# Performance work log

Hardware: AMD Instinct MI355X
Metric: run time of the kernel (lower is better)

Reference implementation:

```python
import jax, jax.numpy as jnp
import numpy as np

B, S, H, OUT = 64, 513, 1024, 128   # batch, seq (incl CLS), hidden, slot labels
T = S - 1                            # subword tokens after dropping [CLS]
P_WORD_START = 0.75                  # avg ~1.33 subwords per word


def setup_inputs() -> dict:
    key = jax.random.key(0)
    k1, k2, k3, k4 = jax.random.split(key, 4)
    hidden_states = jax.random.normal(k1, (B, S, H), jnp.float32)
    W = jax.random.normal(k2, (H, OUT), jnp.float32) * 0.02
    b = jax.random.normal(k3, (OUT,), jnp.float32) * 0.02
    # contiguous, non-decreasing word ids: cumsum of word-start flags
    starts = (jax.random.uniform(k4, (B, T)) < P_WORD_START).astype(jnp.int32)
    starts = starts.at[:, 0].set(1)
    segment_ids = jnp.cumsum(starts, axis=-1) - 1  # [B, T], values in [0, n_words)
    return {"hidden_states": hidden_states, "W": W, "b": b,
            "segment_ids": segment_ids}


def _merge_row(logits, seg):
    # logits: [T, OUT], seg: [T] contiguous non-decreasing word ids
    s = jax.ops.segment_sum(logits, seg, num_segments=T)                    # [T, OUT]
    c = jax.ops.segment_sum(jnp.ones((T,), logits.dtype), seg, num_segments=T)
    mean = s / jnp.maximum(c, 1.0)[:, None]
    # words beyond n_words (empty segments) -> zero padding, as in the original
    return jnp.where(c[:, None] > 0, mean, 0.0)


def reference(hidden_states, W, b, segment_ids):
    x = hidden_states[:, 1:]                       # drop [CLS]; dropout = identity (eval)
    logits = jnp.einsum('bth,ho->bto', x, W) + b   # [B, T, OUT]
    merged = jax.vmap(_merge_row)(logits, segment_ids)  # per-word ragged mean + pad
    return jnp.transpose(merged, (0, 2, 1))        # [B, OUT, T]
```

## Files before the change

### kernel.cpp

```cpp
#include <hip/hip_runtime.h>
#include <hip/hip_bf16.h>

#define B_    64
#define S_    513
#define T_    512
#define H_    1024
#define OUT_  128
#define OWN   64
#define ROWS  96
#define HP    512
#define NKK   16

typedef __attribute__((ext_vector_type(8))) short short8_t;
typedef __attribute__((ext_vector_type(4))) float f32x4;

__device__ inline ushort f2bf(float f) {
    union { float f; unsigned u; } x; x.f = f;
    unsigned r = x.u + 0x7fffu + ((x.u >> 16) & 1u);
    return (ushort)(r >> 16);
}

__global__ __launch_bounds__(256) void wt_kernel(
    const float* __restrict__ W, ushort* __restrict__ Wt)
{
    __shared__ ushort tile[64][65];
    int k0 = blockIdx.x * 64, o0 = blockIdx.y * 64;
    int tid = threadIdx.x;
#pragma unroll
    for (int p = 0; p < 16; ++p) {
        int idx = tid + p * 256;
        int r = idx >> 6, c = idx & 63;
        tile[r][c] = f2bf(W[(size_t)(k0 + r) * OUT_ + o0 + c]);
    }
    __syncthreads();
#pragma unroll
    for (int p = 0; p < 16; ++p) {
        int idx = tid + p * 256;
        int c = idx >> 6, r = idx & 63;
        Wt[(size_t)(o0 + c) * H_ + k0 + r] = tile[r][c];
    }
}

__global__ __launch_bounds__(512, 4) void fused_kernel(
    const float* __restrict__ hs, const ushort* __restrict__ Wt,
    const float* __restrict__ bias, const int* __restrict__ seg,
    float* __restrict__ out)
{
    __shared__ ushort sums[32768];
    __shared__ int sseg[ROWS];
    __shared__ int lcnt[OWN];
    __shared__ int sExt, sSlo;

    int bid  = blockIdx.x;
    int b    = bid >> 3;
    int tile = bid & 7;
    int t0   = tile * OWN;
    int Tl   = (T_ - t0) < ROWS ? (T_ - t0) : ROWS;

    int tid  = threadIdx.x;
    int lane = tid & 63;
    int w    = tid >> 6;
    int wm   = w & 1, wn = w >> 1;
    int l15  = lane & 15, ksl = lane >> 4;

    if (tid < Tl)  sseg[tid] = seg[b * T_ + t0 + tid];
    if (tid < OWN) lcnt[tid] = 0;
    if (tid == 0)  sExt = Tl;
    __syncthreads();
    if (tid == 0) {
        bool start0 = (t0 == 0) || (seg[b * T_ + t0 - 1] != sseg[0]);
        sSlo = sseg[0] + (start0 ? 0 : 1);
    }
    if (tid >= OWN && tid < Tl && sseg[tid] != sseg[tid - 1])
        atomicMin(&sExt, tid);
    __syncthreads();
    int ext  = sExt;
    int s_lo = sSlo;
    int s_hi = sseg[OWN - 1] + 1;
    int ns   = s_hi - s_lo;
    if (tid < ext) {
        int sid = sseg[tid] - s_lo;
        if (sid >= 0) atomicAdd(&lcnt[sid], 1);
    }
    __syncthreads();

    const float* xcol = hs + ((size_t)(b * S_ + 1 + t0)) * H_ + tid;
    const ushort* bp0 = Wt + (size_t)(wn * 32 + l15) * H_ + ksl * 8;
    const ushort* bp1 = bp0 + (size_t)16 * H_;
    int widx   = ((tid >> 3) << 9) + (tid & 7);
    int rbase0 = ksl * 512 + (wm * 32 + l15) * 8;
    int rbase1 = rbase0 + 16 * 8;

    f32x4 acc[2][2];
#pragma unroll
    for (int fm = 0; fm < 2; ++fm)
#pragma unroll
        for (int fn = 0; fn < 2; ++fn) acc[fm][fn] = (f32x4){0.f, 0.f, 0.f, 0.f};

    for (int pass = 0; pass < 2; ++pass) {
        const float* xp = xcol + pass * HP;
        int cur = -1; float racc = 0.f;
        float va[8], vc[8];

        auto LOADC = [&](float (&v)[8], int tb) {
#pragma unroll
            for (int i = 0; i < 8; ++i) {
                int t = tb + i; t = t < Tl ? t : Tl - 1;
                v[i] = xp[(size_t)t * H_];
            }
        };
        auto PROC = [&](float (&v)[8], int tb) {
#pragma unroll
            for (int i = 0; i < 8; ++i) {
                int t = tb + i;
                if (t < ext) {
                    int sid = sseg[t] - s_lo;
                    if (sid >= 0) {
                        if (sid != cur) {
                            if (cur >= 0) sums[widx + (cur << 3)] = f2bf(racc);
                            cur = sid; racc = v[i];
                        } else {
                            racc += v[i];
                        }
                    }
                }
            }
        };

        LOADC(va, 0);
        for (int tb = 0; ; tb += 16) {
            LOADC(vc, tb + 8);
            PROC(va, tb);
            if (tb + 8 >= ext) break;
            LOADC(va, tb + 16);
            PROC(vc, tb + 8);
            if (tb + 16 >= ext) break;
        }
        if (cur >= 0) sums[widx + (cur << 3)] = f2bf(racc);
        __syncthreads();

        const ushort* bq0 = bp0 + pass * HP;
        const ushort* bq1 = bp1 + pass * HP;
        short8_t bfA[2], bfB[2];

        auto LB2 = [&](short8_t (&d)[2], int kk) {
            d[0] = *reinterpret_cast<const short8_t*>(bq0 + kk * 32);
            d[1] = *reinterpret_cast<const short8_t*>(bq1 + kk * 32);
        };
        auto STEP = [&](int kk, short8_t (&bf)[2]) {
            short8_t a0 = *reinterpret_cast<const short8_t*>(&sums[rbase0 + kk * 2048]);
            short8_t a1 = *reinterpret_cast<const short8_t*>(&sums[rbase1 + kk * 2048]);
            acc[0][0] = __builtin_amdgcn_mfma_f32_16x16x32_bf16(a0, bf[0], acc[0][0], 0, 0, 0);
            acc[0][1] = __builtin_amdgcn_mfma_f32_16x16x32_bf16(a0, bf[1], acc[0][1], 0, 0, 0);
            acc[1][0] = __builtin_amdgcn_mfma_f32_16x16x32_bf16(a1, bf[0], acc[1][0], 0, 0, 0);
            acc[1][1] = __builtin_amdgcn_mfma_f32_16x16x32_bf16(a1, bf[1], acc[1][1], 0, 0, 0);
        };

        LB2(bfA, 0);
        for (int kk = 0; kk < NKK; kk += 2) {
            LB2(bfB, kk + 1);
            STEP(kk, bfA);
            if (kk + 2 < NKK) LB2(bfA, kk + 2);
            STEP(kk + 1, bfB);
        }
        __syncthreads();
    }

    int rowb = wm * 32 + ksl * 4;
    float invc[2][4];
#pragma unroll
    for (int fm = 0; fm < 2; ++fm)
#pragma unroll
        for (int r = 0; r < 4; ++r) {
            int row = rowb + fm * 16 + r;
            int cn  = (row < ns) ? lcnt[row] : 1;
            invc[fm][r] = 1.0f / (float)(cn > 0 ? cn : 1);
        }
    float bv0 = bias[wn * 32 + l15];
    float bv1 = bias[wn * 32 + 16 + l15];
#pragma unroll
    for (int fm = 0; fm < 2; ++fm) {
        int row0 = rowb + fm * 16;
#pragma unroll
        for (int fn = 0; fn < 2; ++fn) {
            int o = wn * 32 + fn * 16 + l15;
            float bv = fn ? bv1 : bv0;
            float* dst = out + ((size_t)b * OUT_ + o) * T_ + s_lo + row0;
#pragma unroll
            for (int r = 0; r < 4; ++r)
                if (row0 + r < ns) dst[r] = acc[fm][fn][r] * invc[fm][r] + bv;
        }
    }

    if (tile == 7) {
        int sl = tid & 63, og = tid >> 6;
        for (int o = og; o < OUT_; o += 8)
            for (int s = s_hi + sl; s < T_; s += 64)
                out[((size_t)b * OUT_ + o) * T_ + s] = 0.f;
    }
}

extern "C" void kernel_launch(void* const* d_in, const int* in_sizes, int n_in,
                              void* d_out, int out_size, void* d_ws, size_t ws_size,
                              hipStream_t stream) {
    const float* hs   = (const float*)d_in[0];
    const float* W    = (const float*)d_in[1];
    const float* bias = (const float*)d_in[2];
    const int*   seg  = (const int*)d_in[3];
    float* out = (float*)d_out;

    ushort* Wt = (ushort*)d_ws;

    wt_kernel<<<dim3(H_ / 64, OUT_ / 64), 256, 0, stream>>>(W, Wt);
    fused_kernel<<<B_ * (T_ / OWN), 512, 0, stream>>>(hs, Wt, bias, seg, out);
}
```

Baseline: 67.21 us.

## Split token range across thread groups with float4 loads and single-pass full-K MFMA

```diff
diff --git a/kernel.cpp b/kernel.cpp
--- a/kernel.cpp
+++ b/kernel.cpp
@@ -8,8 +8,8 @@
 #define OUT_  128
 #define OWN   64
 #define ROWS  96
-#define HP    512
-#define NKK   16
+#define GS    32
+#define NKK   32
 
 typedef __attribute__((ext_vector_type(8))) short short8_t;
 typedef __attribute__((ext_vector_type(4))) float f32x4;
@@ -18,6 +18,9 @@
     union { float f; unsigned u; } x; x.f = f;
     unsigned r = x.u + 0x7fffu + ((x.u >> 16) & 1u);
     return (ushort)(r >> 16);
+}
+__device__ inline float bf2f(ushort u) {
+    union { unsigned u; float f; } x; x.u = (unsigned)u << 16; return x.f;
 }
 
 __global__ __launch_bounds__(256) void wt_kernel(
@@ -41,13 +44,14 @@
     }
 }
 
-__global__ __launch_bounds__(512, 4) void fused_kernel(
+__global__ __launch_bounds__(512) void fused_kernel(
     const float* __restrict__ hs, const ushort* __restrict__ Wt,
     const float* __restrict__ bias, const int* __restrict__ seg,
     float* __restrict__ out)
 {
-    __shared__ ushort sums[32768];
-    __shared__ int sseg[ROWS];
+    __shared__ __align__(16) ushort sums[65536];
+    __shared__ __align__(16) float  bnd[H_];
+    __shared__ __align__(16) int sseg[ROWS];
     __shared__ int lcnt[OWN];
     __shared__ int sExt, sSlo;
 
@@ -59,8 +63,7 @@
 
     int tid  = threadIdx.x;
     int lane = tid & 63;
-    int w    = tid >> 6;
-    int wm   = w & 1, wn = w >> 1;
+    int wn   = tid >> 6;
     int l15  = lane & 15, ksl = lane >> 4;
 
     if (tid < Tl)  sseg[tid] = seg[b * T_ + t0 + tid];
@@ -82,113 +85,119 @@
         int sid = sseg[tid] - s_lo;
         if (sid >= 0) atomicAdd(&lcnt[sid], 1);
     }
-    __syncthreads();
-
-    const float* xcol = hs + ((size_t)(b * S_ + 1 + t0)) * H_ + tid;
-    const ushort* bp0 = Wt + (size_t)(wn * 32 + l15) * H_ + ksl * 8;
-    const ushort* bp1 = bp0 + (size_t)16 * H_;
-    int widx   = ((tid >> 3) << 9) + (tid & 7);
-    int rbase0 = ksl * 512 + (wm * 32 + l15) * 8;
-    int rbase1 = rbase0 + 16 * 8;
-
-    f32x4 acc[2][2];
-#pragma unroll
-    for (int fm = 0; fm < 2; ++fm)
-#pragma unroll
-        for (int fn = 0; fn < 2; ++fn) acc[fm][fn] = (f32x4){0.f, 0.f, 0.f, 0.f};
-
-    for (int pass = 0; pass < 2; ++pass) {
-        const float* xp = xcol + pass * HP;
-        int cur = -1; float racc = 0.f;
-        float va[8], vc[8];
-
-        auto LOADC = [&](float (&v)[8], int tb) {
-#pragma unroll
-            for (int i = 0; i < 8; ++i) {
-                int t = tb + i; t = t < Tl ? t : Tl - 1;
-                v[i] = xp[(size_t)t * H_];
-            }
-        };
-        auto PROC = [&](float (&v)[8], int tb) {
-#pragma unroll
-            for (int i = 0; i < 8; ++i) {
-                int t = tb + i;
-                if (t < ext) {
-                    int sid = sseg[t] - s_lo;
-                    if (sid >= 0) {
-                        if (sid != cur) {
-                            if (cur >= 0) sums[widx + (cur << 3)] = f2bf(racc);
-                            cur = sid; racc = v[i];
-                        } else {
-                            racc += v[i];
-                        }
+    int bnd_sid = (sseg[GS] == sseg[GS - 1] && sseg[GS - 1] >= s_lo)
+                    ? sseg[GS - 1] - s_lo : -1;
+
+    int g    = tid >> 8;
+    int col0 = (tid & 255) * 4;
+    int rb   = g * GS;
+    int nt   = g ? (ext - GS) : GS;
+    const float* xp = hs + ((size_t)(b * S_ + 1 + t0)) * H_ + col0;
+    int unit = col0 >> 3, e = col0 & 7;
+
+    float4 racc = {0.f, 0.f, 0.f, 0.f};
+    int cur = -1;
+
+    auto FLUSH = [&](int sid, const float4& r) {
+        if (g == 1 && sid == bnd_sid) {
+            *reinterpret_cast<float4*>(&bnd[col0]) = r;
+        } else {
+            union { ushort u[4]; uint2 v; } pk;
+            pk.u[0] = f2bf(r.x); pk.u[1] = f2bf(r.y);
+            pk.u[2] = f2bf(r.z); pk.u[3] = f2bf(r.w);
+            int el = unit * 512 + (((sid ^ (unit & 7))) << 3) + e;
+            *reinterpret_cast<uint2*>(&sums[el]) = pk.v;
+        }
+    };
+    auto LOADC = [&](float4 (&v)[4], int tb) {
+#pragma unroll
+        for (int i = 0; i < 4; ++i) {
+            int t = rb + tb + i; t = t < Tl ? t : Tl - 1;
+            v[i] = *reinterpret_cast<const float4*>(xp + (size_t)t * H_);
+        }
+    };
+    auto PROC = [&](float4 (&v)[4], int tb) {
+        int4 sd = *reinterpret_cast<const int4*>(&sseg[rb + tb]);
+        int sdv[4] = {sd.x, sd.y, sd.z, sd.w};
+#pragma unroll
+        for (int i = 0; i < 4; ++i) {
+            if (tb + i < nt) {
+                int sid = sdv[i] - s_lo;
+                if (sid >= 0) {
+                    if (sid != cur) {
+                        if (cur >= 0) FLUSH(cur, racc);
+                        cur = sid; racc = v[i];
+                    } else {
+                        racc.x += v[i].x; racc.y += v[i].y;
+                        racc.z += v[i].z; racc.w += v[i].w;
                     }
                 }
             }
-        };
-
-        LOADC(va, 0);
-        for (int tb = 0; ; tb += 16) {
-            LOADC(vc, tb + 8);
-            PROC(va, tb);
-            if (tb + 8 >= ext) break;
-            LOADC(va, tb + 16);
-            PROC(vc, tb + 8);
-            if (tb + 16 >= ext) break;
-        }
-        if (cur >= 0) sums[widx + (cur << 3)] = f2bf(racc);
-        __syncthreads();
-
-        const ushort* bq0 = bp0 + pass * HP;
-        const ushort* bq1 = bp1 + pass * HP;
-        short8_t bfA[2], bfB[2];
-
-        auto LB2 = [&](short8_t (&d)[2], int kk) {
-            d[0] = *reinterpret_cast<const short8_t*>(bq0 + kk * 32);
-            d[1] = *reinterpret_cast<const short8_t*>(bq1 + kk * 32);
-        };
-        auto STEP = [&](int kk, short8_t (&bf)[2]) {
-            short8_t a0 = *reinterpret_cast<const short8_t*>(&sums[rbase0 + kk * 2048]);
-            short8_t a1 = *reinterpret_cast<const short8_t*>(&sums[rbase1 + kk * 2048]);
-            acc[0][0] = __builtin_amdgcn_mfma_f32_16x16x32_bf16(a0, bf[0], acc[0][0], 0, 0, 0);
-            acc[0][1] = __builtin_amdgcn_mfma_f32_16x16x32_bf16(a0, bf[1], acc[0][1], 0, 0, 0);
-            acc[1][0] = __builtin_amdgcn_mfma_f32_16x16x32_bf16(a1, bf[0], acc[1][0], 0, 0, 0);
-            acc[1][1] = __builtin_amdgcn_mfma_f32_16x16x32_bf16(a1, bf[1], acc[1][1], 0, 0, 0);
-        };
-
-        LB2(bfA, 0);
-        for (int kk = 0; kk < NKK; kk += 2) {
-            LB2(bfB, kk + 1);
-            STEP(kk, bfA);
-            if (kk + 2 < NKK) LB2(bfA, kk + 2);
-            STEP(kk + 1, bfB);
-        }
-        __syncthreads();
-    }
-
-    int rowb = wm * 32 + ksl * 4;
-    float invc[2][4];
-#pragma unroll
-    for (int fm = 0; fm < 2; ++fm)
-#pragma unroll
-        for (int r = 0; r < 4; ++r) {
-            int row = rowb + fm * 16 + r;
-            int cn  = (row < ns) ? lcnt[row] : 1;
-            invc[fm][r] = 1.0f / (float)(cn > 0 ? cn : 1);
-        }
-    float bv0 = bias[wn * 32 + l15];
-    float bv1 = bias[wn * 32 + 16 + l15];
-#pragma unroll
-    for (int fm = 0; fm < 2; ++fm) {
-        int row0 = rowb + fm * 16;
-#pragma unroll
-        for (int fn = 0; fn < 2; ++fn) {
-            int o = wn * 32 + fn * 16 + l15;
-            float bv = fn ? bv1 : bv0;
-            float* dst = out + ((size_t)b * OUT_ + o) * T_ + s_lo + row0;
-#pragma unroll
-            for (int r = 0; r < 4; ++r)
-                if (row0 + r < ns) dst[r] = acc[fm][fn][r] * invc[fm][r] + bv;
+        }
+    };
+
+    float4 va[4], vc[4];
+    LOADC(va, 0);
+    for (int tb = 0;; tb += 8) {
+        LOADC(vc, tb + 4);
+        PROC(va, tb);
+        if (tb + 4 >= nt) break;
+        LOADC(va, tb + 8);
+        PROC(vc, tb + 4);
+        if (tb + 8 >= nt) break;
+    }
+    if (cur >= 0) FLUSH(cur, racc);
+    __syncthreads();
+
+    if (bnd_sid >= 0 && tid < 256) {
+        int base = unit * 512 + (((bnd_sid ^ (unit & 7))) << 3) + e;
+#pragma unroll
+        for (int j = 0; j < 4; ++j)
+            sums[base + j] = f2bf(bf2f(sums[base + j]) + bnd[col0 + j]);
+    }
+    __syncthreads();
+
+    const ushort* bp = Wt + (size_t)(wn * 16 + l15) * H_ + ksl * 8;
+    int aE = ksl * 512 + ((l15 ^ ksl) << 3);
+    int aO = ksl * 512 + ((l15 ^ (ksl + 4)) << 3);
+
+    f32x4 acc[4];
+#pragma unroll
+    for (int fm = 0; fm < 4; ++fm) acc[fm] = (f32x4){0.f, 0.f, 0.f, 0.f};
+
+    short8_t bfA, bfB;
+    bfA = *reinterpret_cast<const short8_t*>(bp);
+    for (int kk = 0; kk < NKK; kk += 2) {
+        bfB = *reinterpret_cast<const short8_t*>(bp + (kk + 1) * 32);
+#pragma unroll
+        for (int fm = 0; fm < 4; ++fm) {
+            short8_t a = *reinterpret_cast<const short8_t*>(
+                &sums[aE + fm * 128 + kk * 2048]);
+            acc[fm] = __builtin_amdgcn_mfma_f32_16x16x32_bf16(a, bfA, acc[fm], 0, 0, 0);
+        }
+        if (kk + 2 < NKK)
+            bfA = *reinterpret_cast<const short8_t*>(bp + (kk + 2) * 32);
+#pragma unroll
+        for (int fm = 0; fm < 4; ++fm) {
+            short8_t a = *reinterpret_cast<const short8_t*>(
+                &sums[aO + fm * 128 + (kk + 1) * 2048]);
+            acc[fm] = __builtin_amdgcn_mfma_f32_16x16x32_bf16(a, bfB, acc[fm], 0, 0, 0);
+        }
+    }
+
+    {
+        int o = wn * 16 + l15;
+        float bv = bias[o];
+        float* dstb = out + ((size_t)b * OUT_ + o) * T_ + s_lo;
+#pragma unroll
+        for (int fm = 0; fm < 4; ++fm) {
+            int row0 = fm * 16 + ksl * 4;
+#pragma unroll
+            for (int r = 0; r < 4; ++r) {
+                int row = row0 + r;
+                if (row < ns)
+                    dstb[row] = acc[fm][r] / (float)lcnt[row] + bv;
+            }
         }
     }
 
```

New measurement: 63.34 us. 1.06x faster.
